# Optimization experiments

Measured on AMD Instinct MI355X. Metric: run time of the kernel, lower is better.

Reference implementation:

```python
import jax, jax.numpy as jnp
import numpy as np

B, S, D_MODEL, N_HEADS, D_K, D_V = 2, 2048, 1024, 16, 64, 64
LN_EPS = 1e-5


def setup_inputs() -> dict:
    key = jax.random.key(0)
    ks = jax.random.split(key, 10)
    scale = 1.0 / np.sqrt(D_MODEL)
    inp = {
        "input_Q": jax.random.normal(ks[0], (B, S, D_MODEL), jnp.float32),
        "input_K": jax.random.normal(ks[1], (B, S, D_MODEL), jnp.float32),
        "input_V": jax.random.normal(ks[2], (B, S, D_MODEL), jnp.float32),
        # causal mask (True = masked), as produced by attn_mask() with no pad tokens
        "attn_mask": jnp.broadcast_to(
            jnp.triu(jnp.ones((S, S), dtype=bool), k=1), (B, S, S)
        ),
        # weights stored [in, out] (equivalent to torch Linear weight.T)
        "W_Q": jax.random.normal(ks[3], (D_MODEL, N_HEADS * D_K), jnp.float32) * scale,
        "W_K": jax.random.normal(ks[4], (D_MODEL, N_HEADS * D_K), jnp.float32) * scale,
        "W_V": jax.random.normal(ks[5], (D_MODEL, N_HEADS * D_V), jnp.float32) * scale,
        "W_O": jax.random.normal(ks[6], (N_HEADS * D_V, D_MODEL), jnp.float32) * scale,
        "ln_gamma": jnp.ones((D_MODEL,), jnp.float32),
        "ln_beta": jnp.zeros((D_MODEL,), jnp.float32),
    }
    return inp


def _layernorm(x, gamma, beta):
    mu = jnp.mean(x, axis=-1, keepdims=True)
    var = jnp.var(x, axis=-1, keepdims=True)
    return (x - mu) * jax.lax.rsqrt(var + LN_EPS) * gamma + beta


def reference(input_Q, input_K, input_V, attn_mask, W_Q, W_K, W_V, W_O, ln_gamma, ln_beta):
    b = input_Q.shape[0]
    # projections -> [B, H, S, d]
    Q = (input_Q @ W_Q).reshape(b, -1, N_HEADS, D_K).transpose(0, 2, 1, 3)
    K = (input_K @ W_K).reshape(b, -1, N_HEADS, D_K).transpose(0, 2, 1, 3)
    V = (input_V @ W_V).reshape(b, -1, N_HEADS, D_V).transpose(0, 2, 1, 3)
    scores = jnp.einsum("bhqd,bhkd->bhqk", Q, K) / np.sqrt(D_K)
    scores = jnp.where(attn_mask[:, None, :, :], jnp.float32(-1e9), scores)
    attn = jax.nn.softmax(scores, axis=-1)
    context = jnp.einsum("bhqk,bhkd->bhqd", attn, V)
    context = context.transpose(0, 2, 1, 3).reshape(b, -1, N_HEADS * D_V)
    output = context @ W_O
    out = _layernorm(output + input_Q, ln_gamma, ln_beta)
    return out, attn
```

## Files before the change

### kernel.cpp

```cpp
#include <hip/hip_runtime.h>
#include <stdint.h>

typedef unsigned short u16;
typedef __attribute__((ext_vector_type(8))) short short8;
typedef __attribute__((ext_vector_type(4))) float f32x4;
typedef __attribute__((ext_vector_type(4))) unsigned short u16x4;
typedef __attribute__((ext_vector_type(4))) unsigned int uint4v;

#define MFMA16(a,b,c) __builtin_amdgcn_mfma_f32_16x16x32_bf16((a),(b),(c),0,0,0)

__device__ __forceinline__ void gload16(const void* g, void* l) {
  __builtin_amdgcn_global_load_lds(
      (__attribute__((address_space(1))) void*)(uintptr_t)(g),
      (__attribute__((address_space(3))) void*)(uint32_t)(uintptr_t)(l),
      16, 0, 0);
}

__device__ __forceinline__ u16 f2bf(float x) {
  union { float f; unsigned u; } v; v.f = x;
  unsigned r = v.u + 0x7fffu + ((v.u >> 16) & 1u);
  return (u16)(r >> 16);
}
__device__ __forceinline__ unsigned pack2(float a, float b) {
  return (unsigned)f2bf(a) | ((unsigned)f2bf(b) << 16);
}

__global__ __launch_bounds__(256) void prep_kernel(const float* x0, const float* x1, const float* x2,
                                                   u16* y0, u16* y1, u16* y2,
                                                   const float* w0, const float* w1, const float* w2, const float* w3,
                                                   u16* t0, u16* t1, u16* t2, u16* t3) {
  __shared__ float tile[32][33];
  int z = blockIdx.y;
  if (z < 3) {
    const float* x = (z == 0) ? x0 : ((z == 1) ? x1 : x2);
    u16*         y = (z == 0) ? y0 : ((z == 1) ? y1 : y2);
    size_t i = ((size_t)blockIdx.x * 256 + threadIdx.x) * 4;
    float4 v = *(const float4*)(x + i);
    u16x4 o; o[0] = f2bf(v.x); o[1] = f2bf(v.y); o[2] = f2bf(v.z); o[3] = f2bf(v.w);
    *(u16x4*)(y + i) = o;
  } else {
    if (blockIdx.x >= 1024) return;
    const float* W; u16* T;
    switch (z - 3) {
      case 0:  W = w0; T = t0; break;
      case 1:  W = w1; T = t1; break;
      case 2:  W = w2; T = t2; break;
      default: W = w3; T = t3; break;
    }
    int k0 = (blockIdx.x >> 5) * 32, n0 = (blockIdx.x & 31) * 32;
    int tx = threadIdx.x & 31, ty = threadIdx.x >> 5;
#pragma unroll
    for (int j = 0; j < 4; ++j)
      tile[ty + 8*j][tx] = W[(size_t)(k0 + ty + 8*j) * 1024 + n0 + tx];
    __syncthreads();
#pragma unroll
    for (int j = 0; j < 4; ++j)
      T[(size_t)(n0 + ty + 8*j) * 1024 + k0 + tx] = f2bf(tile[tx][ty + 8*j]);
  }
}

__device__ __forceinline__ void gemm_stage(const u16* A, const u16* BT, int row0, int col0,
                                           int tid, int w, int kt, char* la, char* lb) {
#pragma unroll
  for (int j = 0; j < 2; ++j) {
    int c = j * 256 + tid;
    int mr = c & 127, kc = c >> 7;
    gload16(A  + (size_t)(row0 + mr) * 1024 + kt*32 + kc*8, la + (j*4 + w) * 1024);
    gload16(BT + (size_t)(col0 + mr) * 1024 + kt*32 + kc*8, lb + (j*4 + w) * 1024);
  }
}

__device__ __forceinline__ void gemm_core(const u16* A, const u16* BT, int row0, int col0,
                                          char* ldsA, char* ldsB, f32x4 (&acc)[4][4]) {
  int tid = threadIdx.x, w = tid >> 6, lane = tid & 63;
  int u = lane >> 4, c16 = lane & 15, wr = w >> 1, wc = w & 1;
  gemm_stage(A, BT, row0, col0, tid, w, 0, ldsA, ldsB);
  gemm_stage(A, BT, row0, col0, tid, w, 1, ldsA + 8192, ldsB + 8192);
  int cur = 0;
  for (int kt = 0; kt < 32; ++kt) {
    if (kt < 31) asm volatile("s_waitcnt vmcnt(4)" ::: "memory");
    else         asm volatile("s_waitcnt vmcnt(0)" ::: "memory");
    __builtin_amdgcn_s_barrier();
    asm volatile("" ::: "memory");
    if (kt < 30) {
      int nb = cur + 2; if (nb >= 3) nb -= 3;
      gemm_stage(A, BT, row0, col0, tid, w, kt + 2, ldsA + nb*8192, ldsB + nb*8192);
    }
    __builtin_amdgcn_sched_barrier(0);
    const char* la = ldsA + cur * 8192;
    const char* lb = ldsB + cur * 8192;
    short8 af[4], bv[4];
#pragma unroll
    for (int i = 0; i < 4; ++i) {
      af[i] = *(const short8*)(la + (u*128 + wr*64 + i*16 + c16) * 16);
      bv[i] = *(const short8*)(lb + (u*128 + wc*64 + i*16 + c16) * 16);
    }
#pragma unroll
    for (int i = 0; i < 4; ++i)
#pragma unroll
      for (int n = 0; n < 4; ++n)
        acc[i][n] = MFMA16(af[i], bv[n], acc[i][n]);
    cur = cur + 1; if (cur >= 3) cur = 0;
  }
}

__global__ __launch_bounds__(256) void gemm_qkv(const u16* Xq, const u16* Xk, const u16* Xv,
                                                const u16* WTq, const u16* WTk, const u16* WTv,
                                                u16* Qh, u16* Kh, u16* VhT) {
  __shared__ char ldsA[24576], ldsB[24576];
  int z = blockIdx.z;
  const u16* A  = (z == 0) ? Xq  : ((z == 1) ? Xk  : Xv);
  const u16* BT = (z == 0) ? WTq : ((z == 1) ? WTk : WTv);
  int row0 = blockIdx.x * 128, col0 = blockIdx.y * 128;
  f32x4 acc[4][4] = {};
  gemm_core(A, BT, row0, col0, ldsA, ldsB, acc);
  int tid = threadIdx.x, w = tid >> 6, lane = tid & 63, u = lane >> 4, c16 = lane & 15;
  int wr = w >> 1, wc = w & 1;
#pragma unroll
  for (int i = 0; i < 4; ++i)
#pragma unroll
    for (int n = 0; n < 4; ++n)
#pragma unroll
      for (int r = 0; r < 4; ++r) {
        int row = row0 + wr*64 + i*16 + u*4 + r;
        int colg = col0 + wc*64 + n*16 + c16;
        int b = row >> 11, s = row & 2047;
        int h = colg >> 6, d = colg & 63;
        float v = acc[i][n][r];
        if (z == 0)      Qh[((size_t)(b*16 + h) * 2048 + s) * 64 + d] = f2bf(v * 0.125f);
        else if (z == 1) Kh[((size_t)(b*16 + h) * 2048 + s) * 64 + d] = f2bf(v);
        else             VhT[((size_t)(b*16 + h) * 64 + d) * 2048 + s] = f2bf(v);
      }
}

__global__ __launch_bounds__(256) void gemm_out(const u16* Ctx, const u16* WTo,
                                                const float* resid, float* outF) {
  __shared__ char ldsA[24576], ldsB[24576];
  int row0 = blockIdx.x * 128, col0 = blockIdx.y * 128;
  f32x4 acc[4][4] = {};
  gemm_core(Ctx, WTo, row0, col0, ldsA, ldsB, acc);
  int tid = threadIdx.x, w = tid >> 6, lane = tid & 63, u = lane >> 4, c16 = lane & 15;
  int wr = w >> 1, wc = w & 1;
#pragma unroll
  for (int i = 0; i < 4; ++i)
#pragma unroll
    for (int n = 0; n < 4; ++n)
#pragma unroll
      for (int r = 0; r < 4; ++r) {
        int row = row0 + wr*64 + i*16 + u*4 + r;
        int colg = col0 + wc*64 + n*16 + c16;
        size_t idx = (size_t)row * 1024 + colg;
        outF[idx] = acc[i][n][r] + resid[idx];
      }
}

__device__ __forceinline__ void qk_tile(const char* Kbuf, short8 qf0, short8 qf1,
                                        int cq, int u, int rho, f32x4 (&acc)[4]) {
#pragma unroll
  for (int st = 0; st < 4; ++st) {
    short8 a0 = *(const short8*)(Kbuf + (st*16 + cq) * 128 + ((u*16) ^ rho));
    short8 a1 = *(const short8*)(Kbuf + (st*16 + cq) * 128 + ((64 + u*16) ^ rho));
    acc[st] = MFMA16(a0, qf0, acc[st]);
    acc[st] = MFMA16(a1, qf1, acc[st]);
  }
}

__device__ __forceinline__ void stage_k64(const u16* pan, int kt, char* buf, int tid, int w) {
#pragma unroll
  for (int j = 0; j < 2; ++j) {
    int c = j * 256 + tid;
    int row = c >> 3;
    int cc = (c & 7) ^ (row & 7);
    gload16(pan + (size_t)(kt*64 + row) * 64 + cc*8, buf + (j*4 + w) * 1024);
  }
}
__device__ __forceinline__ void stage_v64(const u16* vpan, int kt, char* buf, int tid, int w) {
#pragma unroll
  for (int j = 0; j < 2; ++j) {
    int c = j * 256 + tid;
    int d = c >> 3;
    int cc = (c & 7) ^ (d & 7);
    gload16(vpan + (size_t)d * 2048 + kt*64 + cc*8, buf + (j*4 + w) * 1024);
  }
}

__device__ __forceinline__ void tile_pass1(const char* Kcur, short8 qf0, short8 qf1,
                                           int q, int q0t, int kt, int ktd_t,
                                           int cq, int u, int rho, float& ls) {
  f32x4 acc[4] = {};
  qk_tile(Kcur, qf0, qf1, cq, u, rho, acc);
  if (kt == ktd_t) {
#pragma unroll
    for (int st = 0; st < 4; ++st)
#pragma unroll
      for (int r = 0; r < 4; ++r) {
        int key = q0t + st*16 + u*4 + r;
        if (key > q) acc[st][r] = -1e30f;
      }
  }
#pragma unroll
  for (int st = 0; st < 4; ++st)
#pragma unroll
    for (int r = 0; r < 4; ++r) ls += __expf(acc[st][r]);
}

__device__ __forceinline__ void tile_pass2(const char* Kcur, const char* Vcur, float* Pw,
                                           short8 qf0, short8 qf1, int q, int q0t, int kt, int ktd_t,
                                           float rl, float* apan, int w, int u, int cq,
                                           int rho, int sw, f32x4 (&ctx)[4]) {
  f32x4 acc[4] = {};
  __builtin_amdgcn_s_setprio(1);
  qk_tile(Kcur, qf0, qf1, cq, u, rho, acc);
  if (kt == ktd_t) {
#pragma unroll
    for (int st = 0; st < 4; ++st)
#pragma unroll
      for (int r = 0; r < 4; ++r) {
        int key = q0t + st*16 + u*4 + r;
        if (key > q) acc[st][r] = -1e30f;
      }
  }
#pragma unroll
  for (int st = 0; st < 4; ++st) {
    f32x4 p;
#pragma unroll
    for (int r = 0; r < 4; ++r) p[r] = __expf(acc[st][r]) * rl;
    *(f32x4*)&Pw[(cq*64 + st*16 + u*4) ^ sw] = p;
  }
  __builtin_amdgcn_sched_barrier(0);
#pragma unroll
  for (int j = 0; j < 4; ++j) {
    int row = j*4 + u;
    f32x4 v = *(const f32x4*)&Pw[(row*64 + cq*4) ^ ((row & 7) << 2)];
    __builtin_nontemporal_store(v,
        (f32x4*)(apan + (size_t)(q0t + w*16 + row) * 2048 + kt*64 + cq*4));
  }
#pragma unroll
  for (int wd = 0; wd < 2; ++wd) {
    int b0 = (cq*64 + wd*32 + u*8) ^ sw;
    f32x4 pa0 = *(const f32x4*)&Pw[b0];
    f32x4 pa1 = *(const f32x4*)&Pw[b0 ^ 4];
    uint4v pk;
    pk[0] = pack2(pa0[0], pa0[1]);
    pk[1] = pack2(pa0[2], pa0[3]);
    pk[2] = pack2(pa1[0], pa1[1]);
    pk[3] = pack2(pa1[2], pa1[3]);
    union { uint4v u4; short8 s8; } cvt; cvt.u4 = pk;
    short8 pa = cvt.s8;
#pragma unroll
    for (int nt = 0; nt < 4; ++nt) {
      short8 vb = *(const short8*)(Vcur + (nt*16 + cq) * 128 + ((wd*64 + u*16) ^ rho));
      ctx[nt] = MFMA16(pa, vb, ctx[nt]);
    }
  }
  __builtin_amdgcn_s_setprio(0);
  __builtin_amdgcn_sched_barrier(0);
}

__global__ __launch_bounds__(256) void attn_fused(const u16* Qh, const u16* Kh, const u16* VhT,
                                                  float* attnO, u16* Ctx) {
  __shared__ char Kl[3][8192];
  __shared__ char Vl[2][8192];
  __shared__ float Pf[4][1024];
  int tid = threadIdx.x, w = tid >> 6, lane = tid & 63;
  int u = lane >> 4, cq = lane & 15;
  int pi = blockIdx.x;
  int bh = blockIdx.y;
  int tlo = pi, thi = 31 - pi;
  int q0lo = tlo * 64, q0hi = thi * 64;
  int qlo = q0lo + w*16 + cq;
  int qhi = q0hi + w*16 + cq;
  int rho = (cq & 7) << 4;
  int sw  = (cq & 7) << 2;
  const u16* Kpan = Kh  + (size_t)bh * (2048 * 64);
  const u16* Vpan = VhT + (size_t)bh * (64 * 2048);
  const u16* Qlo = Qh + ((size_t)bh * 2048 + qlo) * 64;
  const u16* Qhi = Qh + ((size_t)bh * 2048 + qhi) * 64;
  short8 qlo0 = *(const short8*)(Qlo + u*8);
  short8 qlo1 = *(const short8*)(Qlo + 32 + u*8);
  short8 qhi0 = *(const short8*)(Qhi + u*8);
  short8 qhi1 = *(const short8*)(Qhi + 32 + u*8);

  float ls_lo = 0.f, ls_hi = 0.f;
  stage_k64(Kpan, 0, Kl[0], tid, w);
  stage_k64(Kpan, 1, Kl[1], tid, w);
  int cur1 = 0;
  for (int kt = 0; kt <= thi; ++kt) {
    if (kt < thi) asm volatile("s_waitcnt vmcnt(4)" ::: "memory");
    else          asm volatile("s_waitcnt vmcnt(0)" ::: "memory");
    __builtin_amdgcn_s_barrier();
    asm volatile("" ::: "memory");
    if (kt + 2 <= thi) {
      int nb = cur1 + 2; if (nb >= 3) nb -= 3;
      stage_k64(Kpan, kt + 2, Kl[nb], tid, w);
    }
    __builtin_amdgcn_sched_barrier(0);
    __builtin_amdgcn_s_setprio(1);
    tile_pass1(Kl[cur1], qhi0, qhi1, qhi, q0hi, kt, thi, cq, u, rho, ls_hi);
    if (kt <= tlo)
      tile_pass1(Kl[cur1], qlo0, qlo1, qlo, q0lo, kt, tlo, cq, u, rho, ls_lo);
    __builtin_amdgcn_s_setprio(0);
    cur1 = cur1 + 1; if (cur1 >= 3) cur1 = 0;
  }
  ls_lo += __shfl_xor(ls_lo, 16);  ls_lo += __shfl_xor(ls_lo, 32);
  ls_hi += __shfl_xor(ls_hi, 16);  ls_hi += __shfl_xor(ls_hi, 32);
  float rl_lo = 1.f / ls_lo, rl_hi = 1.f / ls_hi;

  asm volatile("" ::: "memory");
  __builtin_amdgcn_s_barrier();
  asm volatile("" ::: "memory");

  f32x4 ctx_lo[4] = {}, ctx_hi[4] = {};
  float* apan = attnO + (size_t)bh * 2048 * 2048;
  float* Pw = Pf[w];
  stage_k64(Kpan, 0, Kl[0], tid, w);
  stage_v64(Vpan, 0, Vl[0], tid, w);
  asm volatile("s_waitcnt vmcnt(0)" ::: "memory");
  __builtin_amdgcn_s_barrier();
  asm volatile("" ::: "memory");
  for (int kt = 0; kt <= thi; ++kt) {
    int cur = kt & 1;
    if (kt < thi) {
      stage_k64(Kpan, kt + 1, Kl[cur ^ 1], tid, w);
      stage_v64(Vpan, kt + 1, Vl[cur ^ 1], tid, w);
    }
    __builtin_amdgcn_sched_barrier(0);
    tile_pass2(Kl[cur], Vl[cur], Pw, qhi0, qhi1, qhi, q0hi, kt, thi,
               rl_hi, apan, w, u, cq, rho, sw, ctx_hi);
    bool lo_act = (kt <= tlo);
    if (lo_act)
      tile_pass2(Kl[cur], Vl[cur], Pw, qlo0, qlo1, qlo, q0lo, kt, tlo,
                 rl_lo, apan, w, u, cq, rho, sw, ctx_lo);
    if (kt < thi) {
      if (lo_act) asm volatile("s_waitcnt vmcnt(8)" ::: "memory");
      else        asm volatile("s_waitcnt vmcnt(4)" ::: "memory");
      __builtin_amdgcn_s_barrier();
      asm volatile("" ::: "memory");
    }
  }

  f32x4 z4 = {};
  for (int kt = tlo + 1; kt < 32; ++kt)
#pragma unroll
    for (int j = 0; j < 4; ++j)
      __builtin_nontemporal_store(z4,
          (f32x4*)(apan + (size_t)(q0lo + w*16 + j*4 + u) * 2048 + kt*64 + cq*4));
  for (int kt = thi + 1; kt < 32; ++kt)
#pragma unroll
    for (int j = 0; j < 4; ++j)
      __builtin_nontemporal_store(z4,
          (f32x4*)(apan + (size_t)(q0hi + w*16 + j*4 + u) * 2048 + kt*64 + cq*4));

  int b = bh >> 4, h = bh & 15;
#pragma unroll
  for (int nt = 0; nt < 4; ++nt)
#pragma unroll
    for (int r = 0; r < 4; ++r) {
      int qr = q0lo + w*16 + u*4 + r;
      Ctx[((size_t)b * 2048 + qr) * 1024 + h*64 + nt*16 + cq] = f2bf(ctx_lo[nt][r]);
    }
#pragma unroll
  for (int nt = 0; nt < 4; ++nt)
#pragma unroll
    for (int r = 0; r < 4; ++r) {
      int qr = q0hi + w*16 + u*4 + r;
      Ctx[((size_t)b * 2048 + qr) * 1024 + h*64 + nt*16 + cq] = f2bf(ctx_hi[nt][r]);
    }
}

__global__ __launch_bounds__(256) void ln_kernel(const float* X, const float* g, const float* b, float* out) {
  int row = blockIdx.x, tid = threadIdx.x;
  float4 v = *(const float4*)(X + (size_t)row * 1024 + tid * 4);
  float s  = v.x + v.y + v.z + v.w;
  float q2 = v.x*v.x + v.y*v.y + v.z*v.z + v.w*v.w;
#pragma unroll
  for (int off = 32; off; off >>= 1) { s += __shfl_xor(s, off); q2 += __shfl_xor(q2, off); }
  __shared__ float red[8];
  int w = tid >> 6, lane = tid & 63;
  if (lane == 0) { red[w] = s; red[4 + w] = q2; }
  __syncthreads();
  s  = red[0] + red[1] + red[2] + red[3];
  q2 = red[4] + red[5] + red[6] + red[7];
  float mean = s * (1.f / 1024.f);
  float var  = q2 * (1.f / 1024.f) - mean * mean;
  float rs   = rsqrtf(var + 1e-5f);
  float4 gv = *(const float4*)(g + tid * 4);
  float4 bv = *(const float4*)(b + tid * 4);
  float4 o;
  o.x = (v.x - mean) * rs * gv.x + bv.x;
  o.y = (v.y - mean) * rs * gv.y + bv.y;
  o.z = (v.z - mean) * rs * gv.z + bv.z;
  o.w = (v.w - mean) * rs * gv.w + bv.w;
  *(float4*)(out + (size_t)row * 1024 + tid * 4) = o;
}

extern "C" void kernel_launch(void* const* d_in, const int* in_sizes, int n_in,
                              void* d_out, int out_size, void* d_ws, size_t ws_size,
                              hipStream_t stream) {
  (void)in_sizes; (void)n_in; (void)out_size; (void)ws_size;
  const float* inQ = (const float*)d_in[0];
  const float* inK = (const float*)d_in[1];
  const float* inV = (const float*)d_in[2];
  const float* Wq  = (const float*)d_in[4];
  const float* Wk  = (const float*)d_in[5];
  const float* Wv  = (const float*)d_in[6];
  const float* Wo  = (const float*)d_in[7];
  const float* gam = (const float*)d_in[8];
  const float* bet = (const float*)d_in[9];
  float* out   = (float*)d_out;
  float* attnO = out + (size_t)4194304;

  char* ws = (char*)d_ws;
  u16*   WTo    = (u16*)ws;
  u16*   Qh     = (u16*)(ws + 2097152);
  u16*   Kh     = (u16*)(ws + 2097152 + (size_t)8388608);
  u16*   VhT    = (u16*)(ws + 2097152 + (size_t)2*8388608);
  u16*   Ctx    = (u16*)(ws + 2097152 + (size_t)3*8388608);
  float* OutLin = (float*)(ws + 2097152 + (size_t)4*8388608);

  u16* Xbq = (u16*)attnO;
  u16* Xbk = Xbq + (size_t)4194304;
  u16* Xbv = Xbk + (size_t)4194304;
  u16* WTq = Xbv + (size_t)4194304;
  u16* WTk = WTq + (size_t)1048576;
  u16* WTv = WTk + (size_t)1048576;

  prep_kernel<<<dim3(4096, 7), 256, 0, stream>>>(inQ, inK, inV, Xbq, Xbk, Xbv,
                                                 Wq, Wk, Wv, Wo, WTq, WTk, WTv, WTo);
  gemm_qkv<<<dim3(32, 8, 3), 256, 0, stream>>>(Xbq, Xbk, Xbv, WTq, WTk, WTv, Qh, Kh, VhT);
  attn_fused<<<dim3(16, 32), 256, 0, stream>>>(Qh, Kh, VhT, attnO, Ctx);
  gemm_out<<<dim3(32, 8), 256, 0, stream>>>(Ctx, WTo, inQ, OutLin);
  ln_kernel<<<4096, 256, 0, stream>>>(OutLin, gam, bet, out);
}
```

Baseline: 269.2 us.

## Interleave zero-fill of masked attention tiles into first softmax pass

Moves the nontemporal zero stores for the fully masked upper-triangle attention tiles out of the kernel tail and spreads them across the first (row-sum) pass, which otherwise writes nothing to global memory. The K staging in that pass drops from triple to double buffering, with prefetch distance reduced to one tile, and the vmcnt waits are retuned to account for the interleaved stores. This is meant to hide the store bandwidth behind compute-bound pass-1 work and free LDS. The risk is less latency hiding for K loads and fragile hand-counted waitcnt values.

```diff
diff --git a/kernel.cpp b/kernel.cpp
--- a/kernel.cpp
+++ b/kernel.cpp
@@ -259,7 +259,7 @@
 
 __global__ __launch_bounds__(256) void attn_fused(const u16* Qh, const u16* Kh, const u16* VhT,
                                                   float* attnO, u16* Ctx) {
-  __shared__ char Kl[3][8192];
+  __shared__ char Kl[2][8192];
   __shared__ char Vl[2][8192];
   __shared__ float Pf[4][1024];
   int tid = threadIdx.x, w = tid >> 6, lane = tid & 63;
@@ -280,27 +280,36 @@
   short8 qlo1 = *(const short8*)(Qlo + 32 + u*8);
   short8 qhi0 = *(const short8*)(Qhi + u*8);
   short8 qhi1 = *(const short8*)(Qhi + 32 + u*8);
+  float* apan = attnO + (size_t)bh * 2048 * 2048;
+  int nlo = 31 - tlo;
+  f32x4 z4 = {};
 
   float ls_lo = 0.f, ls_hi = 0.f;
   stage_k64(Kpan, 0, Kl[0], tid, w);
-  stage_k64(Kpan, 1, Kl[1], tid, w);
-  int cur1 = 0;
   for (int kt = 0; kt <= thi; ++kt) {
-    if (kt < thi) asm volatile("s_waitcnt vmcnt(4)" ::: "memory");
-    else          asm volatile("s_waitcnt vmcnt(0)" ::: "memory");
+    int cur = kt & 1;
+    if (kt == 0 || kt > 16)  asm volatile("s_waitcnt vmcnt(0)" ::: "memory");
+    else if (kt <= 15)       asm volatile("s_waitcnt vmcnt(8)" ::: "memory");
+    else                     asm volatile("s_waitcnt vmcnt(4)" ::: "memory");
     __builtin_amdgcn_s_barrier();
     asm volatile("" ::: "memory");
-    if (kt + 2 <= thi) {
-      int nb = cur1 + 2; if (nb >= 3) nb -= 3;
-      stage_k64(Kpan, kt + 2, Kl[nb], tid, w);
+    if (kt < thi) stage_k64(Kpan, kt + 1, Kl[cur ^ 1], tid, w);
+    int ns = (kt < 15) ? 8 : ((kt == 15) ? 4 : 0);
+    for (int s = 0; s < ns; ++s) {
+      int zidx = kt * 8 + s;
+      int t = zidx >> 2, j = zidx & 3;
+      int ktz, q0t;
+      if (t < nlo) { ktz = tlo + 1 + t;         q0t = q0lo; }
+      else         { ktz = thi + 1 + (t - nlo); q0t = q0hi; }
+      __builtin_nontemporal_store(z4,
+          (f32x4*)(apan + (size_t)(q0t + w*16 + j*4 + u) * 2048 + ktz*64 + cq*4));
     }
     __builtin_amdgcn_sched_barrier(0);
     __builtin_amdgcn_s_setprio(1);
-    tile_pass1(Kl[cur1], qhi0, qhi1, qhi, q0hi, kt, thi, cq, u, rho, ls_hi);
+    tile_pass1(Kl[cur], qhi0, qhi1, qhi, q0hi, kt, thi, cq, u, rho, ls_hi);
     if (kt <= tlo)
-      tile_pass1(Kl[cur1], qlo0, qlo1, qlo, q0lo, kt, tlo, cq, u, rho, ls_lo);
+      tile_pass1(Kl[cur], qlo0, qlo1, qlo, q0lo, kt, tlo, cq, u, rho, ls_lo);
     __builtin_amdgcn_s_setprio(0);
-    cur1 = cur1 + 1; if (cur1 >= 3) cur1 = 0;
   }
   ls_lo += __shfl_xor(ls_lo, 16);  ls_lo += __shfl_xor(ls_lo, 32);
   ls_hi += __shfl_xor(ls_hi, 16);  ls_hi += __shfl_xor(ls_hi, 32);
@@ -311,7 +320,6 @@
   asm volatile("" ::: "memory");
 
   f32x4 ctx_lo[4] = {}, ctx_hi[4] = {};
-  float* apan = attnO + (size_t)bh * 2048 * 2048;
   float* Pw = Pf[w];
   stage_k64(Kpan, 0, Kl[0], tid, w);
   stage_v64(Vpan, 0, Vl[0], tid, w);
@@ -338,18 +346,6 @@
       asm volatile("" ::: "memory");
     }
   }
-
-  f32x4 z4 = {};
-  for (int kt = tlo + 1; kt < 32; ++kt)
-#pragma unroll
-    for (int j = 0; j < 4; ++j)
-      __builtin_nontemporal_store(z4,
-          (f32x4*)(apan + (size_t)(q0lo + w*16 + j*4 + u) * 2048 + kt*64 + cq*4));
-  for (int kt = thi + 1; kt < 32; ++kt)
-#pragma unroll
-    for (int j = 0; j < 4; ++j)
-      __builtin_nontemporal_store(z4,
-          (f32x4*)(apan + (size_t)(q0hi + w*16 + j*4 + u) * 2048 + kt*64 + cq*4));
 
   int b = bh >> 4, h = bh & 15;
 #pragma unroll
```

Result: no change. 270.8 us (+0.6%).

## Remap block indices for XCD-local L2 reuse and vectorize transposed V stores

Applied to the files above, without the earlier changes.

Remaps the block IDs of the QKV GEMM, the output GEMM and the attention kernel so that blocks dispatched round-robin to the same XCD share input rows or the same head. This keeps K/V panels and GEMM A-tiles in that XCD's L2. The transposed V epilogue also now packs four consecutive sequence values into one 8-byte store instead of four scalar 2-byte stores. The remapping relies on the hardware assigning blocks to the 8 XCDs in round-robin order and changes tile scheduling order.

```diff
diff --git a/kernel.cpp b/kernel.cpp
--- a/kernel.cpp
+++ b/kernel.cpp
@@ -8,6 +8,7 @@
 typedef __attribute__((ext_vector_type(4))) unsigned int uint4v;
 
 #define MFMA16(a,b,c) __builtin_amdgcn_mfma_f32_16x16x32_bf16((a),(b),(c),0,0,0)
+#define VWAIT(n) asm volatile("s_waitcnt vmcnt(" #n ")" ::: "memory")
 
 __device__ __forceinline__ void gload16(const void* g, void* l) {
   __builtin_amdgcn_global_load_lds(
@@ -78,8 +79,8 @@
   gemm_stage(A, BT, row0, col0, tid, w, 1, ldsA + 8192, ldsB + 8192);
   int cur = 0;
   for (int kt = 0; kt < 32; ++kt) {
-    if (kt < 31) asm volatile("s_waitcnt vmcnt(4)" ::: "memory");
-    else         asm volatile("s_waitcnt vmcnt(0)" ::: "memory");
+    if (kt < 31) VWAIT(4);
+    else         VWAIT(0);
     __builtin_amdgcn_s_barrier();
     asm volatile("" ::: "memory");
     if (kt < 30) {
@@ -111,32 +112,53 @@
   int z = blockIdx.z;
   const u16* A  = (z == 0) ? Xq  : ((z == 1) ? Xk  : Xv);
   const u16* BT = (z == 0) ? WTq : ((z == 1) ? WTk : WTv);
-  int row0 = blockIdx.x * 128, col0 = blockIdx.y * 128;
+  int id = blockIdx.x + 32 * blockIdx.y;
+  int xcd = id & 7, rank = id >> 3;
+  int row0 = (xcd * 4 + (rank & 3)) * 128;
+  int col0 = (rank >> 2) * 128;
   f32x4 acc[4][4] = {};
   gemm_core(A, BT, row0, col0, ldsA, ldsB, acc);
   int tid = threadIdx.x, w = tid >> 6, lane = tid & 63, u = lane >> 4, c16 = lane & 15;
   int wr = w >> 1, wc = w & 1;
-#pragma unroll
-  for (int i = 0; i < 4; ++i)
-#pragma unroll
-    for (int n = 0; n < 4; ++n)
-#pragma unroll
-      for (int r = 0; r < 4; ++r) {
-        int row = row0 + wr*64 + i*16 + u*4 + r;
+  if (z == 2) {
+#pragma unroll
+    for (int i = 0; i < 4; ++i)
+#pragma unroll
+      for (int n = 0; n < 4; ++n) {
+        int rowb = row0 + wr*64 + i*16 + u*4;
         int colg = col0 + wc*64 + n*16 + c16;
-        int b = row >> 11, s = row & 2047;
+        int b = rowb >> 11, s = rowb & 2047;
         int h = colg >> 6, d = colg & 63;
-        float v = acc[i][n][r];
-        if (z == 0)      Qh[((size_t)(b*16 + h) * 2048 + s) * 64 + d] = f2bf(v * 0.125f);
-        else if (z == 1) Kh[((size_t)(b*16 + h) * 2048 + s) * 64 + d] = f2bf(v);
-        else             VhT[((size_t)(b*16 + h) * 64 + d) * 2048 + s] = f2bf(v);
+        u16x4 pv;
+#pragma unroll
+        for (int r = 0; r < 4; ++r) pv[r] = f2bf(acc[i][n][r]);
+        *(u16x4*)(VhT + ((size_t)(b*16 + h) * 64 + d) * 2048 + s) = pv;
       }
+  } else {
+#pragma unroll
+    for (int i = 0; i < 4; ++i)
+#pragma unroll
+      for (int n = 0; n < 4; ++n)
+#pragma unroll
+        for (int r = 0; r < 4; ++r) {
+          int row = row0 + wr*64 + i*16 + u*4 + r;
+          int colg = col0 + wc*64 + n*16 + c16;
+          int b = row >> 11, s = row & 2047;
+          int h = colg >> 6, d = colg & 63;
+          float v = acc[i][n][r];
+          if (z == 0) Qh[((size_t)(b*16 + h) * 2048 + s) * 64 + d] = f2bf(v * 0.125f);
+          else        Kh[((size_t)(b*16 + h) * 2048 + s) * 64 + d] = f2bf(v);
+        }
+  }
 }
 
 __global__ __launch_bounds__(256) void gemm_out(const u16* Ctx, const u16* WTo,
                                                 const float* resid, float* outF) {
   __shared__ char ldsA[24576], ldsB[24576];
-  int row0 = blockIdx.x * 128, col0 = blockIdx.y * 128;
+  int id = blockIdx.x + 32 * blockIdx.y;
+  int xcd = id & 7, rank = id >> 3;
+  int row0 = (xcd * 4 + (rank & 3)) * 128;
+  int col0 = (rank >> 2) * 128;
   f32x4 acc[4][4] = {};
   gemm_core(Ctx, WTo, row0, col0, ldsA, ldsB, acc);
   int tid = threadIdx.x, w = tid >> 6, lane = tid & 63, u = lane >> 4, c16 = lane & 15;
@@ -264,8 +286,10 @@
   __shared__ float Pf[4][1024];
   int tid = threadIdx.x, w = tid >> 6, lane = tid & 63;
   int u = lane >> 4, cq = lane & 15;
-  int pi = blockIdx.x;
-  int bh = blockIdx.y;
+  int id = blockIdx.x;
+  int xcd = id & 7, rank = id >> 3;
+  int bh = xcd * 4 + (rank >> 4);
+  int pi = rank & 15;
   int tlo = pi, thi = 31 - pi;
   int q0lo = tlo * 64, q0hi = thi * 64;
   int qlo = q0lo + w*16 + cq;
@@ -286,8 +310,8 @@
   stage_k64(Kpan, 1, Kl[1], tid, w);
   int cur1 = 0;
   for (int kt = 0; kt <= thi; ++kt) {
-    if (kt < thi) asm volatile("s_waitcnt vmcnt(4)" ::: "memory");
-    else          asm volatile("s_waitcnt vmcnt(0)" ::: "memory");
+    if (kt < thi) VWAIT(4);
+    else          VWAIT(0);
     __builtin_amdgcn_s_barrier();
     asm volatile("" ::: "memory");
     if (kt + 2 <= thi) {
@@ -315,7 +339,7 @@
   float* Pw = Pf[w];
   stage_k64(Kpan, 0, Kl[0], tid, w);
   stage_v64(Vpan, 0, Vl[0], tid, w);
-  asm volatile("s_waitcnt vmcnt(0)" ::: "memory");
+  VWAIT(0);
   __builtin_amdgcn_s_barrier();
   asm volatile("" ::: "memory");
   for (int kt = 0; kt <= thi; ++kt) {
@@ -332,8 +356,8 @@
       tile_pass2(Kl[cur], Vl[cur], Pw, qlo0, qlo1, qlo, q0lo, kt, tlo,
                  rl_lo, apan, w, u, cq, rho, sw, ctx_lo);
     if (kt < thi) {
-      if (lo_act) asm volatile("s_waitcnt vmcnt(8)" ::: "memory");
-      else        asm volatile("s_waitcnt vmcnt(4)" ::: "memory");
+      if (lo_act) VWAIT(8);
+      else        VWAIT(4);
       __builtin_amdgcn_s_barrier();
       asm volatile("" ::: "memory");
     }
@@ -428,7 +452,7 @@
   prep_kernel<<<dim3(4096, 7), 256, 0, stream>>>(inQ, inK, inV, Xbq, Xbk, Xbv,
                                                  Wq, Wk, Wv, Wo, WTq, WTk, WTv, WTo);
   gemm_qkv<<<dim3(32, 8, 3), 256, 0, stream>>>(Xbq, Xbk, Xbv, WTq, WTk, WTv, Qh, Kh, VhT);
-  attn_fused<<<dim3(16, 32), 256, 0, stream>>>(Qh, Kh, VhT, attnO, Ctx);
+  attn_fused<<<512, 256, 0, stream>>>(Qh, Kh, VhT, attnO, Ctx);
   gemm_out<<<dim3(32, 8), 256, 0, stream>>>(Ctx, WTo, inQ, OutLin);
   ln_kernel<<<4096, 256, 0, stream>>>(OutLin, gam, bet, out);
 }
```

Measured after the change: 254.9 us. 5.3% less time.
